# Kernel optimization log

Hardware: AMD Instinct MI355X
Metric: run time of the kernel (lower is better)

## Reference

```python
import jax, jax.numpy as jnp
import numpy as np

C = 64
CR = C // 8  # reduced channels for Q/K


def _conv1x1(x, W, b):
    # 1x1 conv == per-pixel linear over channels: x [b,c,h,w], W [o,c], b [o]
    return jnp.einsum('bchw,oc->bohw', x, W) + b[None, :, None, None]


def setup_inputs() -> dict:
    key = jax.random.key(0)
    ks = jax.random.split(key, 12)
    b, c, h, w = 8, C, 48, 48
    s = 1.0 / np.sqrt(c)
    inp = {
        'x1': jax.random.normal(ks[0], (b, c, h, w), jnp.float32),
        'x2': jax.random.normal(ks[1], (b, c, h, w), jnp.float32),
        'Wqk1': jax.random.normal(ks[2], (2 * CR, c), jnp.float32) * s,
        'bqk1': jnp.zeros((2 * CR,), jnp.float32),
        'Wqk2': jax.random.normal(ks[3], (2 * CR, c), jnp.float32) * s,
        'bqk2': jnp.zeros((2 * CR,), jnp.float32),
        'Wv1': jax.random.normal(ks[4], (c, c), jnp.float32) * s,
        'bv1': jnp.zeros((c,), jnp.float32),
        'Wv2': jax.random.normal(ks[5], (c, c), jnp.float32) * s,
        'bv2': jnp.zeros((c,), jnp.float32),
        'gamma': jnp.zeros((1,), jnp.float32) + 0.1,  # nonzero so output depends on attn
        'beta': jnp.zeros((1,), jnp.float32) + 0.1,
    }
    return inp


def reference(x1, x2, Wqk1, bqk1, Wqk2, bqk2, Wv1, bv1, Wv2, bv2, gamma, beta):
    b, c, h, w = x1.shape
    n = h * w
    qk1 = _conv1x1(x1, Wqk1, bqk1)
    qk2 = _conv1x1(x2, Wqk2, bqk2)
    q1, k1 = qk1[:, :CR], qk1[:, CR:]
    q2, k2 = qk2[:, :CR], qk2[:, CR:]
    # flatten spatial: [b, cr, n]
    q1 = q1.reshape(b, CR, n); k1 = k1.reshape(b, CR, n)
    q2 = q2.reshape(b, CR, n); k2 = k2.reshape(b, CR, n)
    v1 = _conv1x1(x1, Wv1, bv1).reshape(b, c, n)
    v2 = _conv1x1(x2, Wv2, bv2).reshape(b, c, n)
    # attn[b,i,j] = softmax_j( q[:, :, i] . k[:, :, j] )
    attn1 = jax.nn.softmax(jnp.einsum('bci,bcj->bij', q1, k1), axis=-1)
    attn2 = jax.nn.softmax(jnp.einsum('bci,bcj->bij', q2, k2), axis=-1)
    # out[:, :, j] = sum_i v[:, :, i] * attn[:, i, j]
    o1 = jnp.einsum('bci,bij->bcj', v1, attn2).reshape(b, c, h, w) * gamma + x1
    o2 = jnp.einsum('bci,bij->bcj', v2, attn1).reshape(b, c, h, w) * beta + x2
    return (o1, o2)
```

## Files before the change

kernel.cpp:

```cpp
#include <hip/hip_runtime.h>
#include <hip/hip_bf16.h>

#define NB   8
#define CCH  64
#define CR8  8
#define NPX  2304
#define BCN  (NB*CCH*NPX)
#define LOG2E 1.4426950408889634f

typedef short  short8   __attribute__((ext_vector_type(8)));
typedef unsigned short ushort4t __attribute__((ext_vector_type(4)));
typedef unsigned short ushort8t __attribute__((ext_vector_type(8)));
typedef float  float4t  __attribute__((ext_vector_type(4)));
typedef float  float16t __attribute__((ext_vector_type(16)));

static __device__ __forceinline__ unsigned short bf16bits(float f) {
    __hip_bfloat16 hb = __float2bfloat16(f);
    return *(unsigned short*)&hb;
}

#define WS_QB1 0
#define WS_KB1 (WS_QB1 + 147456)
#define WS_QB2 (WS_KB1 + 147456)
#define WS_KB2 (WS_QB2 + 147456)
#define WS_V1  (WS_KB2 + 147456)
#define WS_V2  (WS_V1 + BCN/2)
#define WS_PD  (WS_V2 + BCN/2)

__global__ __launch_bounds__(256) void proj_kernel(
    const float* __restrict__ x1, const float* __restrict__ x2,
    const float* __restrict__ Wqk1, const float* __restrict__ bqk1,
    const float* __restrict__ Wqk2, const float* __restrict__ bqk2,
    const float* __restrict__ Wv1,  const float* __restrict__ bv1,
    const float* __restrict__ Wv2,  const float* __restrict__ bv2,
    float* __restrict__ ws, float* __restrict__ out)
{
    const int t    = threadIdx.x;
    const int lane = t & 63;
    const int w    = t >> 6;
    const int n16  = lane & 15;
    const int c4   = lane >> 4;
    const int nt   = w & 1;
    const int mh   = w >> 1;
    const int b    = blockIdx.y;
    const int px   = blockIdx.x * 32 + nt * 16 + n16;

    const float* xsb[2];
    xsb[0] = x1 + ((size_t)b * CCH) * NPX + px;
    xsb[1] = x2 + ((size_t)b * CCH) * NPX + px;

    float xr[2][16];
    short8 bfrag[2][2];
    #pragma unroll
    for (int st = 0; st < 2; st++) {
        #pragma unroll
        for (int ch = 0; ch < 2; ch++) {
            #pragma unroll
            for (int j = 0; j < 8; j++)
                xr[st][ch * 8 + j] = xsb[st][(ch * 32 + c4 * 8 + j) * NPX];
            short8 f;
            #pragma unroll
            for (int j = 0; j < 8; j++)
                f[j] = (short)bf16bits(xr[st][ch * 8 + j]);
            bfrag[st][ch] = f;
        }
    }

    if (mh == 0) {
        #pragma unroll
        for (int st = 0; st < 2; st++) {
            float* outs = out + (st ? (size_t)BCN : 0);
            #pragma unroll
            for (int e = 0; e < 16; e++) {
                const int ch = (e >> 3) * 32 + c4 * 8 + (e & 7);
                outs[((size_t)b * CCH + ch) * NPX + px] = xr[st][e];
            }
        }
    }

    float4t acc[5];
    #pragma unroll
    for (int mt = 0; mt < 5; mt++) { acc[mt][0]=0.f; acc[mt][1]=0.f; acc[mt][2]=0.f; acc[mt][3]=0.f; }

    #pragma unroll
    for (int mt = 0; mt < 5; mt++) {
        const int mi  = mh * 5 + mt;
        const int isqk = (mi < 2);
        const int st  = isqk ? (mi & 1) : (mi >= 6);
        const float* Wb;
        int rowbase;
        if (isqk) { Wb = (mi == 0) ? Wqk1 : Wqk2; rowbase = 0; }
        else      { Wb = (mi >= 6) ? Wv2 : Wv1; rowbase = (mi - (mi >= 6 ? 6 : 2)) * 16; }
        const float* wrow = Wb + (size_t)(rowbase + n16) * 64 + c4 * 8;

        const short8 bf0 = st ? bfrag[1][0] : bfrag[0][0];
        const short8 bf1 = st ? bfrag[1][1] : bfrag[0][1];

        #pragma unroll
        for (int ch = 0; ch < 2; ch++) {
            const float4 a0 = *(const float4*)(wrow + ch * 32);
            const float4 a1 = *(const float4*)(wrow + ch * 32 + 4);
            short8 af;
            af[0] = (short)bf16bits(a0.x); af[1] = (short)bf16bits(a0.y);
            af[2] = (short)bf16bits(a0.z); af[3] = (short)bf16bits(a0.w);
            af[4] = (short)bf16bits(a1.x); af[5] = (short)bf16bits(a1.y);
            af[6] = (short)bf16bits(a1.z); af[7] = (short)bf16bits(a1.w);
            acc[mt] = __builtin_amdgcn_mfma_f32_16x16x32_bf16(
                af, ch ? bf1 : bf0, acc[mt], 0, 0, 0);
        }
    }

    #pragma unroll
    for (int mt = 0; mt < 5; mt++) {
        const int mi = mh * 5 + mt;
        if (mi < 2) {
            const int st = mi & 1;
            const float* bqk = st ? bqk2 : bqk1;
            unsigned short* qb = (unsigned short*)(ws + (st ? WS_QB2 : WS_QB1));
            unsigned short* kb = (unsigned short*)(ws + (st ? WS_KB2 : WS_KB1));
            const size_t rbase = (size_t)(b * NPX + px) * 16;
            #pragma unroll
            for (int r = 0; r < 4; r++) {
                const int oc = c4 * 4 + r;
                const float val = acc[mt][r] + bqk[oc];
                if (oc < 8)
                    qb[rbase + oc] = bf16bits(val * LOG2E);
                else
                    kb[rbase + (oc - 8)] = bf16bits(val);
            }
            ushort8t z;
            #pragma unroll
            for (int e = 0; e < 8; e++) z[e] = 0;
            if (c4 == 0) *(ushort8t*)(qb + rbase + 8) = z;
            if (c4 == 2) *(ushort8t*)(kb + rbase + 8) = z;
        } else {
            const int st = (mi >= 6);
            const int vt_ = mi - (st ? 6 : 2);
            const float* bv = st ? bv2 : bv1;
            unsigned short* v = (unsigned short*)(ws + (st ? WS_V2 : WS_V1));
            #pragma unroll
            for (int r = 0; r < 4; r++) {
                const int oc = vt_ * 16 + c4 * 4 + r;
                const float val = acc[mt][r] + bv[oc];
                v[((size_t)b * CCH + oc) * NPX + px] = bf16bits(val);
            }
        }
    }
}

__global__ __launch_bounds__(256) void stats_kernel(float* __restrict__ ws)
{
    const int t  = threadIdx.x;
    const int w  = t >> 6;
    const int n  = t & 31;
    const int h  = (t & 63) >> 5;
    const int jsb = blockIdx.x;
    const int iq  = blockIdx.y;
    const int ab  = blockIdx.z;
    const int b   = ab & 7;
    const int a   = ab >> 3;

    const unsigned short* qb = (const unsigned short*)(ws + (a ? WS_QB2 : WS_QB1));
    const unsigned short* kb = (const unsigned short*)(ws + (a ? WS_KB2 : WS_KB1));
    float* pd = ws + WS_PD;

    __shared__ float red[4][576];

    const int j = jsb * 128 + w * 32 + n;
    const short8 kfrag = *(const short8*)(kb + (size_t)(b * NPX + j) * 16 + h * 8);

    for (int ib = 0; ib < 18; ib++) {
        const int i = iq * 576 + ib * 32 + n;
        const short8 qfrag = *(const short8*)(qb + (size_t)(b * NPX + i) * 16 + h * 8);
        float16t acc = {};
        acc = __builtin_amdgcn_mfma_f32_32x32x16_bf16(kfrag, qfrag, acc, 0, 0, 0);
        float ssum = 0.f;
        #pragma unroll
        for (int r = 0; r < 16; r++) ssum += exp2f(acc[r]);
        ssum += __shfl_xor(ssum, 32);
        if (h == 0) red[w][ib * 32 + n] = ssum;
    }
    __syncthreads();
    for (int idx = t; idx < 576; idx += 256)
        pd[((size_t)ab * 18 + jsb) * NPX + iq * 576 + idx] =
            red[0][idx] + red[1][idx] + red[2][idx] + red[3][idx];
}

__global__ __launch_bounds__(256) void merge_scale(float* __restrict__ ws)
{
    const float* pd = ws + WS_PD;
    const int idx = blockIdx.x * 256 + threadIdx.x;
    const int i  = idx % NPX;
    const int ab = idx / NPX;
    const int b  = ab & 7;
    const int a  = ab >> 3;
    float d = 0.f;
    #pragma unroll
    for (int c = 0; c < 18; c++)
        d += pd[((size_t)ab * 18 + c) * NPX + i];
    const float r = 1.0f / d;

    unsigned short* vv = (unsigned short*)(ws + (a ? WS_V1 : WS_V2));
    const size_t base = (size_t)b * CCH * NPX + i;
    #pragma unroll 8
    for (int c = 0; c < 64; c++) {
        const size_t ix = base + (size_t)c * NPX;
        __hip_bfloat16 hb;
        *(unsigned short*)&hb = vv[ix];
        hb = __float2bfloat16(__bfloat162float(hb) * r);
        vv[ix] = *(unsigned short*)&hb;
    }
}

__global__ __launch_bounds__(256) void out_kernel(
    const float* __restrict__ gamma, const float* __restrict__ beta,
    const float* __restrict__ ws, float* __restrict__ out)
{
    const int t  = threadIdx.x;
    const int jt = blockIdx.x;
    const int b  = blockIdx.y;
    const int z  = blockIdx.z;
    const int o  = z >> 1;
    const int ihalf = z & 1;

    const int a = o ? 0 : 1;
    const unsigned short* qb = (const unsigned short*)(ws + (a ? WS_QB2 : WS_QB1));
    const unsigned short* kb = (const unsigned short*)(ws + (a ? WS_KB2 : WS_KB1));
    const unsigned short* v  = (const unsigned short*)(ws + (o ? WS_V2 : WS_V1));
    const float  scale = o ? beta[0] : gamma[0];

    __shared__ unsigned short vt[64][72];
    __shared__ unsigned short pt[64][132];

    const int j0   = jt * 64;
    const int lane = t & 63;
    const int w    = t >> 6;
    const int n    = lane & 31;
    const int h    = lane >> 5;
    const int jh   = w & 1;
    const int ihq  = w >> 1;
    const int cbase = 32 * (w & 1);
    const int jbase = 32 * (w >> 1);

    const short8 kfrag = *(const short8*)(kb + (size_t)(b * NPX + j0 + 32 * jh + n) * 16 + h * 8);

    float16t oacc = {};

    for (int it = 0; it < 18; it++) {
        const int i0 = ihalf * 1152 + it * 64;
        __syncthreads();

        #pragma unroll
        for (int r = 0; r < 2; r++) {
            const int seg = t + r * 256;
            const int c = seg >> 3, s8 = seg & 7;
            *(float4*)&vt[c][s8 * 8] =
                *(const float4*)(v + ((size_t)b * CCH + c) * NPX + i0 + s8 * 8);
        }

        const short8 qfrag = *(const short8*)(qb + (size_t)(b * NPX + i0 + 32 * ihq + n) * 16 + h * 8);
        float16t sc = {};
        sc = __builtin_amdgcn_mfma_f32_32x32x16_bf16(qfrag, kfrag, sc, 0, 0, 0);

        #pragma unroll
        for (int gq = 0; gq < 4; gq++) {
            const int ibl = 32 * ihq + 8 * gq + 4 * h;
            ushort4t pk;
            pk[0] = bf16bits(exp2f(sc[gq * 4 + 0]));
            pk[1] = bf16bits(exp2f(sc[gq * 4 + 1]));
            pk[2] = bf16bits(exp2f(sc[gq * 4 + 2]));
            pk[3] = bf16bits(exp2f(sc[gq * 4 + 3]));
            *(ushort4t*)&pt[32 * jh + n][ibl] = pk;
        }
        __syncthreads();

        #pragma unroll
        for (int kk = 0; kk < 4; kk++) {
            const short8 afrag = *(const short8*)&vt[cbase + n][kk * 16 + h * 8];
            const short8 bfrag = *(const short8*)&pt[jbase + n][kk * 16 + h * 8];
            oacc = __builtin_amdgcn_mfma_f32_32x32x16_bf16(afrag, bfrag, oacc, 0, 0, 0);
        }
    }

    const size_t outoff = o ? (size_t)BCN : 0;
    #pragma unroll
    for (int r = 0; r < 16; r++) {
        const int row = (r & 3) + 8 * (r >> 2) + 4 * h;
        const int c = cbase + row;
        const size_t gidx = ((size_t)b * CCH + c) * NPX + j0 + jbase + n;
        atomicAdd(&out[outoff + gidx], oacc[r] * scale);
    }
}

extern "C" void kernel_launch(void* const* d_in, const int* in_sizes, int n_in,
                              void* d_out, int out_size, void* d_ws, size_t ws_size,
                              hipStream_t stream)
{
    const float* x1   = (const float*)d_in[0];
    const float* x2   = (const float*)d_in[1];
    const float* Wqk1 = (const float*)d_in[2];
    const float* bqk1 = (const float*)d_in[3];
    const float* Wqk2 = (const float*)d_in[4];
    const float* bqk2 = (const float*)d_in[5];
    const float* Wv1  = (const float*)d_in[6];
    const float* bv1  = (const float*)d_in[7];
    const float* Wv2  = (const float*)d_in[8];
    const float* bv2  = (const float*)d_in[9];
    const float* gamma = (const float*)d_in[10];
    const float* beta  = (const float*)d_in[11];
    float* out = (float*)d_out;
    float* ws  = (float*)d_ws;

    proj_kernel<<<dim3(72, 8), 256, 0, stream>>>(
        x1, x2, Wqk1, bqk1, Wqk2, bqk2, Wv1, bv1, Wv2, bv2, ws, out);
    stats_kernel<<<dim3(18, 4, 16), 256, 0, stream>>>(ws);
    merge_scale<<<dim3(144), 256, 0, stream>>>(ws);
    out_kernel<<<dim3(36, 8, 4), 256, 0, stream>>>(gamma, beta, ws, out);
}
```

Baseline: 169.1 us.

## Fold softmax normalizer into padded QK dot product instead of rescaling V

```diff
diff --git a/kernel.cpp b/kernel.cpp
--- a/kernel.cpp
+++ b/kernel.cpp
@@ -128,11 +128,12 @@
                 else
                     kb[rbase + (oc - 8)] = bf16bits(val);
             }
-            ushort8t z;
-            #pragma unroll
-            for (int e = 0; e < 8; e++) z[e] = 0;
-            if (c4 == 0) *(ushort8t*)(qb + rbase + 8) = z;
-            if (c4 == 2) *(ushort8t*)(kb + rbase + 8) = z;
+            ushort8t zq, zk;
+            #pragma unroll
+            for (int e = 0; e < 8; e++) { zq[e] = 0; zk[e] = 0; }
+            zk[0] = 0x3F80; zk[1] = 0x3F80;
+            if (c4 == 0) *(ushort8t*)(qb + rbase + 8) = zq;
+            if (c4 == 2) *(ushort8t*)(kb + rbase + 8) = zk;
         } else {
             const int st = (mi >= 6);
             const int vt_ = mi - (st ? 6 : 2);
@@ -174,9 +175,15 @@
         const short8 qfrag = *(const short8*)(qb + (size_t)(b * NPX + i) * 16 + h * 8);
         float16t acc = {};
         acc = __builtin_amdgcn_mfma_f32_32x32x16_bf16(kfrag, qfrag, acc, 0, 0, 0);
-        float ssum = 0.f;
-        #pragma unroll
-        for (int r = 0; r < 16; r++) ssum += exp2f(acc[r]);
+        float s0 = 0.f, s1 = 0.f, s2 = 0.f, s3 = 0.f;
+        #pragma unroll
+        for (int r = 0; r < 4; r++) {
+            s0 += exp2f(acc[4 * r + 0]);
+            s1 += exp2f(acc[4 * r + 1]);
+            s2 += exp2f(acc[4 * r + 2]);
+            s3 += exp2f(acc[4 * r + 3]);
+        }
+        float ssum = (s0 + s1) + (s2 + s3);
         ssum += __shfl_xor(ssum, 32);
         if (h == 0) red[w][ib * 32 + n] = ssum;
     }
@@ -186,7 +193,7 @@
             red[0][idx] + red[1][idx] + red[2][idx] + red[3][idx];
 }
 
-__global__ __launch_bounds__(256) void merge_scale(float* __restrict__ ws)
+__global__ __launch_bounds__(256) void merge_fold(float* __restrict__ ws)
 {
     const float* pd = ws + WS_PD;
     const int idx = blockIdx.x * 256 + threadIdx.x;
@@ -198,18 +205,16 @@
     #pragma unroll
     for (int c = 0; c < 18; c++)
         d += pd[((size_t)ab * 18 + c) * NPX + i];
-    const float r = 1.0f / d;
-
-    unsigned short* vv = (unsigned short*)(ws + (a ? WS_V1 : WS_V2));
-    const size_t base = (size_t)b * CCH * NPX + i;
-    #pragma unroll 8
-    for (int c = 0; c < 64; c++) {
-        const size_t ix = base + (size_t)c * NPX;
-        __hip_bfloat16 hb;
-        *(unsigned short*)&hb = vv[ix];
-        hb = __float2bfloat16(__bfloat162float(hb) * r);
-        vv[ix] = *(unsigned short*)&hb;
-    }
+    const float m = -__log2f(d);
+
+    const unsigned short mh = bf16bits(m);
+    __hip_bfloat16 hb; *(unsigned short*)&hb = mh;
+    const unsigned short ml = bf16bits(m - __bfloat162float(hb));
+
+    unsigned short* qb = (unsigned short*)(ws + (a ? WS_QB2 : WS_QB1));
+    const size_t rbase = (size_t)(b * NPX + i) * 16;
+    qb[rbase + 8] = mh;
+    qb[rbase + 9] = ml;
 }
 
 __global__ __launch_bounds__(256) void out_kernel(
@@ -314,6 +319,6 @@
     proj_kernel<<<dim3(72, 8), 256, 0, stream>>>(
         x1, x2, Wqk1, bqk1, Wqk2, bqk2, Wv1, bv1, Wv2, bv2, ws, out);
     stats_kernel<<<dim3(18, 4, 16), 256, 0, stream>>>(ws);
-    merge_scale<<<dim3(144), 256, 0, stream>>>(ws);
+    merge_fold<<<dim3(144), 256, 0, stream>>>(ws);
     out_kernel<<<dim3(36, 8, 4), 256, 0, stream>>>(gamma, beta, ws, out);
 }
```

Result: faster. 164.1 us (-3.0%).
